# Kernel tuning notes

Measured on AMD Instinct MI355X. Metric: run time of the kernel, lower is better.

## Reference

```python
import jax, jax.numpy as jnp
import numpy as np

N_NODES = 100000
N_EDGES = 8192
DEG = 32                      # nodes per hyperedge
NNZ = N_EDGES * DEG
D_IN = 128
D_HID = 128
D_EDGE = 64
EPS = 1e-5


def _batchnorm(x, g, b):
    # normalize per-feature over the batch (dim 0), as a BatchNorm1d in train mode
    mu = jnp.mean(x, axis=0)
    var = jnp.var(x, axis=0)
    return (x - mu) * jax.lax.rsqrt(var + EPS) * g + b


def _hconv(x, src, eid, w, W, b):
    # hypergraph conv: linear -> node->edge weighted sum -> edge->node weighted sum
    h = x @ W + b                                          # [N, Dout]
    m = jax.ops.segment_sum(w[:, None] * h[src], eid, num_segments=N_EDGES)
    out = jax.ops.segment_sum(w[:, None] * m[eid], src, num_segments=N_NODES)
    return out


def setup_inputs() -> dict:
    key = jax.random.key(0)
    ks = jax.random.split(key, 20)
    src = jax.random.randint(ks[0], (NNZ,), 0, N_NODES)
    eid = jnp.arange(NNZ) // DEG                          # every edge id appears DEG times
    edge_index = jnp.stack([src, eid]).astype(jnp.int64)
    s = lambda k, sh, f: jax.random.normal(k, sh, jnp.float32) * f
    return {
        "x": s(ks[1], (N_NODES, D_IN), 1.0),
        "edge_index": edge_index,
        "edge_weight": jax.random.uniform(ks[2], (NNZ,), jnp.float32),
        "edge_features": s(ks[3], (N_EDGES, D_EDGE), 1.0),
        "adj": jax.random.uniform(ks[4], (N_EDGES, N_EDGES), jnp.float32) / N_EDGES,
        "T": 2,
        "norm1_g": jnp.ones((D_IN,), jnp.float32),
        "norm1_b": jnp.zeros((D_IN,), jnp.float32),
        "norm2_g": jnp.ones((D_EDGE,), jnp.float32),
        "norm2_b": jnp.zeros((D_EDGE,), jnp.float32),
        "W1": s(ks[5], (D_IN, D_HID), 0.05),
        "b1": jnp.zeros((D_HID,), jnp.float32),
        "W2": s(ks[6], (D_HID, D_HID), 0.05),
        "b2": jnp.zeros((D_HID,), jnp.float32),
        "Wn": s(ks[7], (D_HID, D_HID), 0.05),
        "We": s(ks[8], (D_EDGE, D_HID), 0.05),
        "Wg": s(ks[9], (D_HID, D_HID), 0.05),
        "cls_w1": s(ks[10], (D_HID, 16), 0.1),
        "cls_b1": jnp.zeros((16,), jnp.float32),
        "cls_w2": s(ks[11], (16, 2), 0.1),
        "cls_b2": jnp.zeros((2,), jnp.float32),
    }


def reference(x, edge_index, edge_weight, edge_features, adj, T,
              norm1_g, norm1_b, norm2_g, norm2_b,
              W1, b1, W2, b2, Wn, We, Wg,
              cls_w1, cls_b1, cls_w2, cls_b2):
    src, eid = edge_index[0], edge_index[1]
    x = _batchnorm(x, norm1_g, norm1_b)
    x = _hconv(x, src, eid, edge_weight, W1, b1)
    x = _hconv(x, src, eid, edge_weight, W2, b2)
    x = jax.nn.relu(x)
    # aggregate_node_features (mean over nodes incident to each hyperedge) —
    # the per-edge Python loop becomes one fused segment reduce
    s = jax.ops.segment_sum(x[src], eid, num_segments=N_EDGES)           # [E, D]
    cnt = jax.ops.segment_sum(jnp.ones_like(eid, jnp.float32), eid, num_segments=N_EDGES)
    node_features = s / jnp.maximum(cnt, 1.0)[:, None]
    ef = _batchnorm(edge_features, norm2_g, norm2_b)
    # edge-level graph convolution with T propagation steps over edge-edge adj
    h = jax.nn.relu(node_features @ Wn + ef @ We)
    for _ in range(T):
        h = jax.nn.relu(adj @ (h @ Wg))
    # classifier head
    out = jax.nn.relu(h @ cls_w1 + cls_b1) @ cls_w2 + cls_b2             # [E, 2]
    return out
```

## Files before the change

kernel.cpp:

```cpp
#include <hip/hip_runtime.h>

#define N_NODESC 100000
#define N_EDGESC 8192
#define DEGC 32
#define DF 128
#define DEF 64
#define EPSV 1e-5f
#define KSPLIT 8
#define KSLICE (N_EDGESC / KSPLIT)

#define NCVT 16384
#define NXST 400
#define NEST 64

typedef __attribute__((ext_vector_type(8))) short short8;
typedef __attribute__((ext_vector_type(4))) float f32x4;
typedef __attribute__((ext_vector_type(8))) unsigned short ushort8;
typedef __attribute__((ext_vector_type(4))) unsigned short u16x4;

typedef const void __attribute__((address_space(1)))* gptr_t;
typedef void __attribute__((address_space(3)))* lptr_t;

struct EW { int e; float w; };

__device__ __forceinline__ unsigned short f2bf(float x) {
    union { float f; unsigned u; } v; v.f = x;
    unsigned r = v.u + 0x7fffu + ((v.u >> 16) & 1u);
    return (unsigned short)(r >> 16);
}

__global__ __launch_bounds__(256) void fused_pre(const float* __restrict__ x,
                                                 const float* __restrict__ ef,
                                                 const int* __restrict__ src,
                                                 const float* __restrict__ ew,
                                                 const float* __restrict__ adj,
                                                 unsigned short* __restrict__ adjbf,
                                                 float* __restrict__ stats,
                                                 int* __restrict__ cnt,
                                                 EW* __restrict__ ewpk) {
    const int b = blockIdx.x;
    if (b < NCVT) {
        const size_t base4 = (size_t)b * 1024;
        const f32x4* in4 = (const f32x4*)adj + base4;
        u16x4* out4 = (u16x4*)adjbf + base4;
        f32x4 a[4];
        #pragma unroll
        for (int k = 0; k < 4; ++k) a[k] = in4[threadIdx.x + k * 256];
        #pragma unroll
        for (int k = 0; k < 4; ++k) {
            u16x4 r;
            r[0] = f2bf(a[k][0]); r[1] = f2bf(a[k][1]);
            r[2] = f2bf(a[k][2]); r[3] = f2bf(a[k][3]);
            out4[threadIdx.x + k * 256] = r;
        }
        return;
    }
    const int bs = b - NCVT;
    if (bs >= NXST + NEST) {
        int i = (bs - NXST - NEST) * 256 + threadIdx.x;
        int n = src[i];
        int pos = atomicAdd(&cnt[n], 1);
        if (pos < DEGC) {
            EW t; t.e = i >> 5; t.w = ew[i];
            ewpk[(size_t)n * DEGC + pos] = t;
        }
        return;
    }
    __shared__ f32x4 ls[256], lq[256];
    if (bs < NXST) {
        const int q = threadIdx.x & 31, rg = threadIdx.x >> 5;
        f32x4 s = {0.f, 0.f, 0.f, 0.f}, s2 = {0.f, 0.f, 0.f, 0.f};
        for (int r = bs * 8 + rg; r < N_NODESC; r += NXST * 8) {
            f32x4 v = *(const f32x4*)&x[(size_t)r * DF + q * 4];
            s += v; s2 += v * v;
        }
        ls[threadIdx.x] = s; lq[threadIdx.x] = s2;
        __syncthreads();
        if (threadIdx.x < 32) {
            #pragma unroll
            for (int g = 1; g < 8; ++g) { s += ls[threadIdx.x + g * 32]; s2 += lq[threadIdx.x + g * 32]; }
            #pragma unroll
            for (int i = 0; i < 4; ++i) {
                atomicAdd(&stats[q * 4 + i], s[i]);
                atomicAdd(&stats[128 + q * 4 + i], s2[i]);
            }
        }
    } else {
        const int bb = bs - NXST;
        const int q = threadIdx.x & 15, rg = threadIdx.x >> 4;
        f32x4 s = {0.f, 0.f, 0.f, 0.f}, s2 = {0.f, 0.f, 0.f, 0.f};
        for (int r = bb * 16 + rg; r < N_EDGESC; r += NEST * 16) {
            f32x4 v = *(const f32x4*)&ef[(size_t)r * DEF + q * 4];
            s += v; s2 += v * v;
        }
        ls[threadIdx.x] = s; lq[threadIdx.x] = s2;
        __syncthreads();
        if (threadIdx.x < 16) {
            #pragma unroll
            for (int g = 1; g < 16; ++g) { s += ls[threadIdx.x + g * 16]; s2 += lq[threadIdx.x + g * 16]; }
            #pragma unroll
            for (int i = 0; i < 4; ++i) {
                atomicAdd(&stats[512 + q * 4 + i], s[i]);
                atomicAdd(&stats[576 + q * 4 + i], s2[i]);
            }
        }
    }
}

__global__ void finalize_both(const float* __restrict__ stats,
                              const float* __restrict__ g1, const float* __restrict__ b1,
                              const float* __restrict__ g2, const float* __restrict__ b2,
                              float* __restrict__ ssx, float* __restrict__ sse) {
    int t = threadIdx.x;
    if (t < 128) {
        float mean = stats[t] / (float)N_NODESC;
        float var = stats[128 + t] / (float)N_NODESC - mean * mean;
        float sc = g1[t] * rsqrtf(var + EPSV);
        ssx[t] = sc;
        ssx[128 + t] = b1[t] - mean * sc;
    } else {
        int f = t - 128;
        float mean = stats[512 + f] / (float)N_EDGESC;
        float var = stats[576 + f] / (float)N_EDGESC - mean * mean;
        float sc = g2[f] * rsqrtf(var + EPSV);
        sse[f] = sc;
        sse[64 + f] = b2[f] - mean * sc;
    }
}

__global__ __launch_bounds__(256) void node_apply(const float* __restrict__ m,
                                                  const int* __restrict__ cnt,
                                                  const EW* __restrict__ ewpk,
                                                  float* __restrict__ out) {
    const int n = blockIdx.x * 2 + (threadIdx.x >> 7);
    const int f = threadIdx.x & 127;
    if (n >= N_NODESC) return;
    int d = cnt[n];
    if (d <= 0) return;
    d = min(d, DEGC);
    const EW* q = ewpk + (size_t)n * DEGC;
    float acc = 0.f;
    for (int p = 0; p < d; ++p) {
        EW t = q[p];
        acc += t.w * m[(size_t)t.e * DF + f];
    }
    out[(size_t)n * DF + f] = acc;
}

template<bool WEIGHTED, bool AFFINE, bool RELU, bool WRITE_SW>
__global__ __launch_bounds__(128) void gather_k(const float* __restrict__ X,
                                                const float* __restrict__ w,
                                                const int* __restrict__ src,
                                                const float* __restrict__ scale,
                                                const float* __restrict__ shift,
                                                float* __restrict__ out,
                                                float* __restrict__ swout,
                                                float mul) {
    const int e = blockIdx.x, f = threadIdx.x;
    const int base = e * DEGC;
    float acc = 0.f, sw = 0.f;
    #pragma unroll
    for (int j = 0; j < DEGC; ++j) {
        int n = src[base + j];
        float wj = WEIGHTED ? w[base + j] : 1.f;
        float v = X[(size_t)n * DF + f];
        if (RELU) v = fmaxf(v, 0.f);
        acc += wj * v;
        sw += wj;
    }
    float r = acc;
    if (AFFINE) r = acc * scale[f] + sw * shift[f];
    out[(size_t)e * DF + f] = r * mul;
    if (WRITE_SW && f == 0) swout[e] = sw;
}

template<int K1, int K2, int NSLICE, bool RELU_IN, bool RELU_OUT, bool BIAS>
__global__ __launch_bounds__(256) void egemm(const float* __restrict__ A1, const float* __restrict__ W1p,
                                             const float* __restrict__ A2, const float* __restrict__ W2p,
                                             const float* __restrict__ sc2, const float* __restrict__ sh2,
                                             const float* __restrict__ bias, const float* __restrict__ swv,
                                             float* __restrict__ C) {
    constexpr int P1 = K1 + 4;
    constexpr int K2c = (K2 > 0) ? K2 : 1;
    constexpr int P2 = K2c + 4;
    constexpr size_t SLSTR = (size_t)N_EDGESC * K1;
    __shared__ float wt1[DF * P1];
    __shared__ float a1c[32 * K1];
    __shared__ float wt2[(K2 > 0) ? DF * P2 : 1];
    __shared__ float a2c[(K2 > 0) ? 32 * K2c : 1];

    const int tid = threadIdx.x;
    const int r0 = blockIdx.x * 32;

    for (int idx = tid; idx < K1 * DF; idx += 256) {
        int k = idx >> 7, c = idx & 127;
        wt1[c * P1 + k] = W1p[idx];
    }
    for (int idx = tid; idx < 32 * K1; idx += 256) {
        float v;
        if constexpr (NSLICE > 1) {
            v = 0.f;
            #pragma unroll
            for (int s = 0; s < NSLICE; ++s) v += A1[s * SLSTR + (size_t)r0 * K1 + idx];
        } else {
            v = A1[(size_t)r0 * K1 + idx];
        }
        if (RELU_IN) v = fmaxf(v, 0.f);
        a1c[idx] = v;
    }
    if constexpr (K2 > 0) {
        for (int idx = tid; idx < K2 * DF; idx += 256) {
            int k = idx >> 7, c = idx & 127;
            wt2[c * P2 + k] = W2p[idx];
        }
        for (int idx = tid; idx < 32 * K2; idx += 256) {
            int k = idx % K2;
            a2c[idx] = A2[(size_t)r0 * K2 + idx] * sc2[k] + sh2[k];
        }
    }
    __syncthreads();

    const int cg = tid & 31, rg = tid >> 5;
    float acc[4][4];
    if constexpr (BIAS) {
        float bl[4], sl[4];
        #pragma unroll
        for (int j = 0; j < 4; ++j) bl[j] = bias[cg * 4 + j];
        #pragma unroll
        for (int i = 0; i < 4; ++i) sl[i] = swv[r0 + rg * 4 + i];
        #pragma unroll
        for (int i = 0; i < 4; ++i)
            #pragma unroll
            for (int j = 0; j < 4; ++j) acc[i][j] = sl[i] * bl[j];
    } else {
        #pragma unroll
        for (int i = 0; i < 4; ++i)
            #pragma unroll
            for (int j = 0; j < 4; ++j) acc[i][j] = 0.f;
    }

    #pragma unroll 4
    for (int k4 = 0; k4 < K1; k4 += 4) {
        f32x4 av[4], wv[4];
        #pragma unroll
        for (int i = 0; i < 4; ++i) av[i] = *(const f32x4*)&a1c[(rg * 4 + i) * K1 + k4];
        #pragma unroll
        for (int j = 0; j < 4; ++j) wv[j] = *(const f32x4*)&wt1[(cg * 4 + j) * P1 + k4];
        #pragma unroll
        for (int i = 0; i < 4; ++i)
            #pragma unroll
            for (int j = 0; j < 4; ++j)
                #pragma unroll
                for (int q = 0; q < 4; ++q) acc[i][j] += av[i][q] * wv[j][q];
    }
    if constexpr (K2 > 0) {
        #pragma unroll 4
        for (int k4 = 0; k4 < K2; k4 += 4) {
            f32x4 av[4], wv[4];
            #pragma unroll
            for (int i = 0; i < 4; ++i) av[i] = *(const f32x4*)&a2c[(rg * 4 + i) * K2c + k4];
            #pragma unroll
            for (int j = 0; j < 4; ++j) wv[j] = *(const f32x4*)&wt2[(cg * 4 + j) * P2 + k4];
            #pragma unroll
            for (int i = 0; i < 4; ++i)
                #pragma unroll
                for (int j = 0; j < 4; ++j)
                    #pragma unroll
                    for (int q = 0; q < 4; ++q) acc[i][j] += av[i][q] * wv[j][q];
        }
    }

    #pragma unroll
    for (int i = 0; i < 4; ++i) {
        f32x4 o;
        #pragma unroll
        for (int j = 0; j < 4; ++j) {
            float v = acc[i][j];
            if (RELU_OUT) v = fmaxf(v, 0.f);
            o[j] = v;
        }
        *(f32x4*)&C[(size_t)(r0 + rg * 4 + i) * DF + cg * 4] = o;
    }
}

__global__ __launch_bounds__(256) void transp_cvt(const float* __restrict__ Y,
                                                  unsigned short* __restrict__ Yt) {
    __shared__ float t[32][33];
    const int r0 = blockIdx.x * 32, c0 = blockIdx.y * 32;
    const int tc = threadIdx.x & 31, tr = threadIdx.x >> 5;
    #pragma unroll
    for (int i = 0; i < 4; ++i)
        t[tr + i * 8][tc] = Y[(size_t)(r0 + tr + i * 8) * DF + c0 + tc];
    __syncthreads();
    #pragma unroll
    for (int i = 0; i < 4; ++i) {
        int c = tr + i * 8;
        Yt[(size_t)(c0 + c) * N_EDGESC + r0 + tc] = f2bf(t[tc][c]);
    }
}

__global__ __launch_bounds__(256, 2) void adj_gemm(const unsigned short* __restrict__ A,
                                                   const unsigned short* __restrict__ Bt,
                                                   float* __restrict__ H) {
    __shared__ unsigned short sA[2][128 * 64];
    __shared__ unsigned short sB[2][128 * 64];
    const int tid = threadIdx.x;
    const int lane = tid & 63, wave = tid >> 6;
    const int mb = blockIdx.x & 63, ks = blockIdx.x >> 6;
    const size_t m0 = (size_t)mb * 128;
    const int k0 = ks * KSLICE;
    const int wm = wave >> 1, wn = wave & 1;
    float* __restrict__ Hs = H + (size_t)ks * (N_EDGESC * DF);

    f32x4 acc[4][4];
    #pragma unroll
    for (int i = 0; i < 4; ++i)
        #pragma unroll
        for (int j = 0; j < 4; ++j) acc[i][j] = 0.f;

    auto stage = [&](int buf, int kc) {
        #pragma unroll
        for (int i = 0; i < 4; ++i) {
            int slot = i * 256 + wave * 64 + lane;
            int row = slot >> 3, ch = slot & 7;
            int sc = (ch ^ (row & 7)) << 3;
            const unsigned short* ga = A + (m0 + row) * (size_t)N_EDGESC + kc + sc;
            const unsigned short* gb = Bt + (size_t)row * N_EDGESC + kc + sc;
            unsigned short* la = &sA[buf][(i * 256 + wave * 64) * 8];
            unsigned short* lb = &sB[buf][(i * 256 + wave * 64) * 8];
            __builtin_amdgcn_global_load_lds((gptr_t)ga, (lptr_t)la, 16, 0, 0);
            __builtin_amdgcn_global_load_lds((gptr_t)gb, (lptr_t)lb, 16, 0, 0);
        }
    };

    stage(0, k0);
    int cur = 0;
    for (int c = 0; c < KSLICE / 64; ++c) {
        __syncthreads();
        if (c + 1 < KSLICE / 64) stage(cur ^ 1, k0 + (c + 1) * 64);
        #pragma unroll
        for (int kk = 0; kk < 2; ++kk) {
            short8 af[4], bv[4];
            const int chb = kk * 4 + (lane >> 4);
            #pragma unroll
            for (int mf = 0; mf < 4; ++mf) {
                int row = wm * 64 + mf * 16 + (lane & 15);
                af[mf] = *(const short8*)&sA[cur][(row * 8 + (chb ^ (row & 7))) * 8];
            }
            #pragma unroll
            for (int nf = 0; nf < 4; ++nf) {
                int row = wn * 64 + nf * 16 + (lane & 15);
                bv[nf] = *(const short8*)&sB[cur][(row * 8 + (chb ^ (row & 7))) * 8];
            }
            #pragma unroll
            for (int mf = 0; mf < 4; ++mf)
                #pragma unroll
                for (int nf = 0; nf < 4; ++nf)
                    acc[mf][nf] = __builtin_amdgcn_mfma_f32_16x16x32_bf16(af[mf], bv[nf], acc[mf][nf], 0, 0, 0);
        }
        cur ^= 1;
    }

    #pragma unroll
    for (int mf = 0; mf < 4; ++mf)
        #pragma unroll
        for (int nf = 0; nf < 4; ++nf)
            #pragma unroll
            for (int r = 0; r < 4; ++r) {
                size_t row = m0 + wm * 64 + mf * 16 + (lane >> 4) * 4 + r;
                int col = wn * 64 + nf * 16 + (lane & 15);
                Hs[row * DF + col] = acc[mf][nf][r];
            }
}

__global__ __launch_bounds__(256) void classifier_k(const float* __restrict__ H,
                                                    const float* __restrict__ w1, const float* __restrict__ b1,
                                                    const float* __restrict__ w2, const float* __restrict__ b2,
                                                    float* __restrict__ out) {
    constexpr size_t SLSTR = (size_t)N_EDGESC * DF;
    __shared__ float hl[16 * DF];
    __shared__ float w1l[DF * 16];
    __shared__ float hid[16 * 16];
    const int tid = threadIdx.x;
    const int e0 = blockIdx.x * 16;
    for (int idx = tid; idx < 16 * DF; idx += 256) {
        float v = 0.f;
        #pragma unroll
        for (int s = 0; s < KSPLIT; ++s) v += H[s * SLSTR + (size_t)e0 * DF + idx];
        hl[idx] = fmaxf(v, 0.f);
    }
    for (int idx = tid; idx < DF * 16; idx += 256) w1l[idx] = w1[idx];
    __syncthreads();
    {
        int el = tid >> 4, j = tid & 15;
        float a = b1[j];
        for (int k = 0; k < DF; ++k) a += hl[el * DF + k] * w1l[k * 16 + j];
        hid[el * 16 + j] = fmaxf(a, 0.f);
    }
    __syncthreads();
    if (tid < 32) {
        int e = tid >> 1, o = tid & 1;
        float s = b2[o];
        for (int jj = 0; jj < 16; ++jj) s += hid[e * 16 + jj] * w2[jj * 2 + o];
        out[(size_t)(e0 + e) * 2 + o] = s;
    }
}

extern "C" void kernel_launch(void* const* d_in, const int* in_sizes, int n_in,
                              void* d_out, int out_size, void* d_ws, size_t ws_size,
                              hipStream_t stream) {
    const float* x   = (const float*)d_in[0];
    const int*  src  = (const int*)d_in[1];
    const float* ew  = (const float*)d_in[2];
    const float* ef  = (const float*)d_in[3];
    const float* adj = (const float*)d_in[4];
    const float* n1g = (const float*)d_in[6];
    const float* n1b = (const float*)d_in[7];
    const float* n2g = (const float*)d_in[8];
    const float* n2b = (const float*)d_in[9];
    const float* W1  = (const float*)d_in[10];
    const float* b1  = (const float*)d_in[11];
    const float* W2  = (const float*)d_in[12];
    const float* b2  = (const float*)d_in[13];
    const float* Wn  = (const float*)d_in[14];
    const float* We  = (const float*)d_in[15];
    const float* Wg  = (const float*)d_in[16];
    const float* cw1 = (const float*)d_in[17];
    const float* cb1 = (const float*)d_in[18];
    const float* cw2 = (const float*)d_in[19];
    const float* cb2 = (const float*)d_in[20];
    float* out = (float*)d_out;

    float* stats  = (float*)d_ws;
    float* ssx    = stats + 256;
    float* sse    = stats + 640;
    float* sw     = stats + 1024;
    int*   cnt    = (int*)(sw + 8192);
    EW*    ewpk   = (EW*)(cnt + N_NODESC);
    float* EB0    = (float*)(ewpk + (size_t)N_NODESC * DEGC);
    float* EB1    = EB0 + (size_t)N_EDGESC * DF;
    float* HS     = EB1 + (size_t)N_EDGESC * DF;
    float* NODES  = HS + (size_t)KSPLIT * N_EDGESC * DF;
    unsigned short* yT    = (unsigned short*)(NODES + (size_t)N_NODESC * DF);
    unsigned short* adjbf = yT + (size_t)DF * N_EDGESC;

    (void)hipMemsetAsync(stats, 0, (1024 + 8192) * sizeof(float) + N_NODESC * sizeof(int), stream);

    fused_pre<<<NCVT + NXST + NEST + (N_EDGESC * DEGC) / 256, 256, 0, stream>>>(
        x, ef, src, ew, adj, adjbf, stats, cnt, ewpk);
    finalize_both<<<1, 192, 0, stream>>>(stats, n1g, n1b, n2g, n2b, ssx, sse);

    gather_k<true, true, false, true><<<N_EDGESC, 128, 0, stream>>>(x, ew, src, ssx, ssx + 128, EB0, sw, 1.f);
    egemm<128, 0, 1, false, false, true><<<256, 256, 0, stream>>>(EB0, W1, nullptr, nullptr, nullptr, nullptr, b1, sw, EB1);
    node_apply<<<N_NODESC / 2, 256, 0, stream>>>(EB1, cnt, ewpk, NODES);

    gather_k<true, false, false, false><<<N_EDGESC, 128, 0, stream>>>(NODES, ew, src, nullptr, nullptr, EB0, nullptr, 1.f);
    egemm<128, 0, 1, false, false, true><<<256, 256, 0, stream>>>(EB0, W2, nullptr, nullptr, nullptr, nullptr, b2, sw, EB1);
    node_apply<<<N_NODESC / 2, 256, 0, stream>>>(EB1, cnt, ewpk, NODES);

    gather_k<false, false, true, false><<<N_EDGESC, 128, 0, stream>>>(NODES, nullptr, src, nullptr, nullptr, EB0, nullptr, 1.f / DEGC);

    egemm<128, 64, 1, false, true, false><<<256, 256, 0, stream>>>(EB0, Wn, ef, We, sse, sse + 64, nullptr, nullptr, EB1);

    egemm<128, 0, 1, false, false, false><<<256, 256, 0, stream>>>(EB1, Wg, nullptr, nullptr, nullptr, nullptr, nullptr, nullptr, EB0);
    transp_cvt<<<dim3(256, 4), 256, 0, stream>>>(EB0, yT);
    adj_gemm<<<64 * KSPLIT, 256, 0, stream>>>(adjbf, yT, HS);
    egemm<128, 0, KSPLIT, true, false, false><<<256, 256, 0, stream>>>(HS, Wg, nullptr, nullptr, nullptr, nullptr, nullptr, nullptr, EB0);
    transp_cvt<<<dim3(256, 4), 256, 0, stream>>>(EB0, yT);
    adj_gemm<<<64 * KSPLIT, 256, 0, stream>>>(adjbf, yT, HS);

    classifier_k<<<N_EDGESC / 16, 256, 0, stream>>>(HS, cw1, cb1, cw2, cb2, out);
}
```

Before: 492.3 us.

## Spread adj bf16 conversion across gather/node kernels and fold BN finalize into consumers

The 16384-block fp32-to-bf16 conversion of the adjacency matrix is moved out of the up-front pre-pass. It is split into five chunks of 3277 blocks, each prepended to one of the memory-latency-bound gather_k and node_apply launches so it can overlap with their gathers. The finalize_both kernel is removed: BN scale and shift are computed inline in gather_k for x and in egemm for edge features. gather_k also handles two edges per 256-thread block. This saves one launch and tries to hide conversion bandwidth, at the cost of mixing streaming and gather blocks in each launch.

```diff
diff --git a/kernel.cpp b/kernel.cpp
--- a/kernel.cpp
+++ b/kernel.cpp
@@ -9,7 +9,8 @@
 #define KSPLIT 8
 #define KSLICE (N_EDGESC / KSPLIT)
 
-#define NCVT 16384
+#define NCVT_TOT 16384
+#define CVS 3277
 #define NXST 400
 #define NEST 64
 
@@ -29,35 +30,34 @@
     return (unsigned short)(r >> 16);
 }
 
-__global__ __launch_bounds__(256) void fused_pre(const float* __restrict__ x,
+__device__ __forceinline__ void cvt_block(int cb, const float* __restrict__ adj,
+                                          unsigned short* __restrict__ adjbf) {
+    if (cb >= NCVT_TOT) return;
+    const size_t base4 = (size_t)cb * 1024;
+    const f32x4* in4 = (const f32x4*)adj + base4;
+    u16x4* out4 = (u16x4*)adjbf + base4;
+    f32x4 a[4];
+    #pragma unroll
+    for (int k = 0; k < 4; ++k) a[k] = in4[threadIdx.x + k * 256];
+    #pragma unroll
+    for (int k = 0; k < 4; ++k) {
+        u16x4 r;
+        r[0] = f2bf(a[k][0]); r[1] = f2bf(a[k][1]);
+        r[2] = f2bf(a[k][2]); r[3] = f2bf(a[k][3]);
+        out4[threadIdx.x + k * 256] = r;
+    }
+}
+
+__global__ __launch_bounds__(256) void pre_small(const float* __restrict__ x,
                                                  const float* __restrict__ ef,
                                                  const int* __restrict__ src,
                                                  const float* __restrict__ ew,
-                                                 const float* __restrict__ adj,
-                                                 unsigned short* __restrict__ adjbf,
                                                  float* __restrict__ stats,
                                                  int* __restrict__ cnt,
                                                  EW* __restrict__ ewpk) {
     const int b = blockIdx.x;
-    if (b < NCVT) {
-        const size_t base4 = (size_t)b * 1024;
-        const f32x4* in4 = (const f32x4*)adj + base4;
-        u16x4* out4 = (u16x4*)adjbf + base4;
-        f32x4 a[4];
-        #pragma unroll
-        for (int k = 0; k < 4; ++k) a[k] = in4[threadIdx.x + k * 256];
-        #pragma unroll
-        for (int k = 0; k < 4; ++k) {
-            u16x4 r;
-            r[0] = f2bf(a[k][0]); r[1] = f2bf(a[k][1]);
-            r[2] = f2bf(a[k][2]); r[3] = f2bf(a[k][3]);
-            out4[threadIdx.x + k * 256] = r;
-        }
-        return;
-    }
-    const int bs = b - NCVT;
-    if (bs >= NXST + NEST) {
-        int i = (bs - NXST - NEST) * 256 + threadIdx.x;
+    if (b >= NXST + NEST) {
+        int i = (b - NXST - NEST) * 256 + threadIdx.x;
         int n = src[i];
         int pos = atomicAdd(&cnt[n], 1);
         if (pos < DEGC) {
@@ -67,10 +67,10 @@
         return;
     }
     __shared__ f32x4 ls[256], lq[256];
-    if (bs < NXST) {
+    if (b < NXST) {
         const int q = threadIdx.x & 31, rg = threadIdx.x >> 5;
         f32x4 s = {0.f, 0.f, 0.f, 0.f}, s2 = {0.f, 0.f, 0.f, 0.f};
-        for (int r = bs * 8 + rg; r < N_NODESC; r += NXST * 8) {
+        for (int r = b * 8 + rg; r < N_NODESC; r += NXST * 8) {
             f32x4 v = *(const f32x4*)&x[(size_t)r * DF + q * 4];
             s += v; s2 += v * v;
         }
@@ -86,7 +86,7 @@
             }
         }
     } else {
-        const int bb = bs - NXST;
+        const int bb = b - NXST;
         const int q = threadIdx.x & 15, rg = threadIdx.x >> 4;
         f32x4 s = {0.f, 0.f, 0.f, 0.f}, s2 = {0.f, 0.f, 0.f, 0.f};
         for (int r = bb * 16 + rg; r < N_EDGESC; r += NEST * 16) {
@@ -107,32 +107,17 @@
     }
 }
 
-__global__ void finalize_both(const float* __restrict__ stats,
-                              const float* __restrict__ g1, const float* __restrict__ b1,
-                              const float* __restrict__ g2, const float* __restrict__ b2,
-                              float* __restrict__ ssx, float* __restrict__ sse) {
-    int t = threadIdx.x;
-    if (t < 128) {
-        float mean = stats[t] / (float)N_NODESC;
-        float var = stats[128 + t] / (float)N_NODESC - mean * mean;
-        float sc = g1[t] * rsqrtf(var + EPSV);
-        ssx[t] = sc;
-        ssx[128 + t] = b1[t] - mean * sc;
-    } else {
-        int f = t - 128;
-        float mean = stats[512 + f] / (float)N_EDGESC;
-        float var = stats[576 + f] / (float)N_EDGESC - mean * mean;
-        float sc = g2[f] * rsqrtf(var + EPSV);
-        sse[f] = sc;
-        sse[64 + f] = b2[f] - mean * sc;
-    }
-}
-
 __global__ __launch_bounds__(256) void node_apply(const float* __restrict__ m,
                                                   const int* __restrict__ cnt,
                                                   const EW* __restrict__ ewpk,
-                                                  float* __restrict__ out) {
-    const int n = blockIdx.x * 2 + (threadIdx.x >> 7);
+                                                  float* __restrict__ out,
+                                                  const float* __restrict__ adj,
+                                                  unsigned short* __restrict__ adjbf,
+                                                  int cvtBase) {
+    int b = blockIdx.x;
+    if (b < CVS) { cvt_block(cvtBase + b, adj, adjbf); return; }
+    b -= CVS;
+    const int n = b * 2 + (threadIdx.x >> 7);
     const int f = threadIdx.x & 127;
     if (n >= N_NODESC) return;
     int d = cnt[n];
@@ -148,15 +133,30 @@
 }
 
 template<bool WEIGHTED, bool AFFINE, bool RELU, bool WRITE_SW>
-__global__ __launch_bounds__(128) void gather_k(const float* __restrict__ X,
+__global__ __launch_bounds__(256) void gather_k(const float* __restrict__ X,
                                                 const float* __restrict__ w,
                                                 const int* __restrict__ src,
-                                                const float* __restrict__ scale,
-                                                const float* __restrict__ shift,
+                                                const float* __restrict__ stats,
+                                                const float* __restrict__ g1,
+                                                const float* __restrict__ b1,
                                                 float* __restrict__ out,
                                                 float* __restrict__ swout,
-                                                float mul) {
-    const int e = blockIdx.x, f = threadIdx.x;
+                                                float mul,
+                                                const float* __restrict__ adj,
+                                                unsigned short* __restrict__ adjbf,
+                                                int cvtBase) {
+    int b = blockIdx.x;
+    if (b < CVS) { cvt_block(cvtBase + b, adj, adjbf); return; }
+    b -= CVS;
+    const int e = b * 2 + (threadIdx.x >> 7);
+    const int f = threadIdx.x & 127;
+    float scale = 1.f, shift = 0.f;
+    if (AFFINE) {
+        float mean = stats[f] / (float)N_NODESC;
+        float var = stats[128 + f] / (float)N_NODESC - mean * mean;
+        scale = g1[f] * rsqrtf(var + EPSV);
+        shift = b1[f] - mean * scale;
+    }
     const int base = e * DEGC;
     float acc = 0.f, sw = 0.f;
     #pragma unroll
@@ -169,7 +169,7 @@
         sw += wj;
     }
     float r = acc;
-    if (AFFINE) r = acc * scale[f] + sw * shift[f];
+    if (AFFINE) r = acc * scale + sw * shift;
     out[(size_t)e * DF + f] = r * mul;
     if (WRITE_SW && f == 0) swout[e] = sw;
 }
@@ -177,7 +177,8 @@
 template<int K1, int K2, int NSLICE, bool RELU_IN, bool RELU_OUT, bool BIAS>
 __global__ __launch_bounds__(256) void egemm(const float* __restrict__ A1, const float* __restrict__ W1p,
                                              const float* __restrict__ A2, const float* __restrict__ W2p,
-                                             const float* __restrict__ sc2, const float* __restrict__ sh2,
+                                             const float* __restrict__ statsE, const float* __restrict__ g2,
+                                             const float* __restrict__ b2v, float cntE,
                                              const float* __restrict__ bias, const float* __restrict__ swv,
                                              float* __restrict__ C) {
     constexpr int P1 = K1 + 4;
@@ -188,9 +189,21 @@
     __shared__ float a1c[32 * K1];
     __shared__ float wt2[(K2 > 0) ? DF * P2 : 1];
     __shared__ float a2c[(K2 > 0) ? 32 * K2c : 1];
+    __shared__ float sseL[(K2 > 0) ? 2 * K2c : 1];
 
     const int tid = threadIdx.x;
     const int r0 = blockIdx.x * 32;
+
+    if constexpr (K2 > 0) {
+        if (tid < K2) {
+            float mean = statsE[tid] / cntE;
+            float var = statsE[K2 + tid] / cntE - mean * mean;
+            float sc = g2[tid] * rsqrtf(var + EPSV);
+            sseL[tid] = sc;
+            sseL[K2 + tid] = b2v[tid] - mean * sc;
+        }
+        __syncthreads();
+    }
 
     for (int idx = tid; idx < K1 * DF; idx += 256) {
         int k = idx >> 7, c = idx & 127;
@@ -215,7 +228,7 @@
         }
         for (int idx = tid; idx < 32 * K2; idx += 256) {
             int k = idx % K2;
-            a2c[idx] = A2[(size_t)r0 * K2 + idx] * sc2[k] + sh2[k];
+            a2c[idx] = A2[(size_t)r0 * K2 + idx] * sseL[k] + sseL[K2 + k];
         }
     }
     __syncthreads();
@@ -432,8 +445,6 @@
     float* out = (float*)d_out;
 
     float* stats  = (float*)d_ws;
-    float* ssx    = stats + 256;
-    float* sse    = stats + 640;
     float* sw     = stats + 1024;
     int*   cnt    = (int*)(sw + 8192);
     EW*    ewpk   = (EW*)(cnt + N_NODESC);
@@ -446,26 +457,33 @@
 
     (void)hipMemsetAsync(stats, 0, (1024 + 8192) * sizeof(float) + N_NODESC * sizeof(int), stream);
 
-    fused_pre<<<NCVT + NXST + NEST + (N_EDGESC * DEGC) / 256, 256, 0, stream>>>(
-        x, ef, src, ew, adj, adjbf, stats, cnt, ewpk);
-    finalize_both<<<1, 192, 0, stream>>>(stats, n1g, n1b, n2g, n2b, ssx, sse);
-
-    gather_k<true, true, false, true><<<N_EDGESC, 128, 0, stream>>>(x, ew, src, ssx, ssx + 128, EB0, sw, 1.f);
-    egemm<128, 0, 1, false, false, true><<<256, 256, 0, stream>>>(EB0, W1, nullptr, nullptr, nullptr, nullptr, b1, sw, EB1);
-    node_apply<<<N_NODESC / 2, 256, 0, stream>>>(EB1, cnt, ewpk, NODES);
-
-    gather_k<true, false, false, false><<<N_EDGESC, 128, 0, stream>>>(NODES, ew, src, nullptr, nullptr, EB0, nullptr, 1.f);
-    egemm<128, 0, 1, false, false, true><<<256, 256, 0, stream>>>(EB0, W2, nullptr, nullptr, nullptr, nullptr, b2, sw, EB1);
-    node_apply<<<N_NODESC / 2, 256, 0, stream>>>(EB1, cnt, ewpk, NODES);
-
-    gather_k<false, false, true, false><<<N_EDGESC, 128, 0, stream>>>(NODES, nullptr, src, nullptr, nullptr, EB0, nullptr, 1.f / DEGC);
-
-    egemm<128, 64, 1, false, true, false><<<256, 256, 0, stream>>>(EB0, Wn, ef, We, sse, sse + 64, nullptr, nullptr, EB1);
-
-    egemm<128, 0, 1, false, false, false><<<256, 256, 0, stream>>>(EB1, Wg, nullptr, nullptr, nullptr, nullptr, nullptr, nullptr, EB0);
+    pre_small<<<NXST + NEST + (N_EDGESC * DEGC) / 256, 256, 0, stream>>>(
+        x, ef, src, ew, stats, cnt, ewpk);
+
+    gather_k<true, true, false, true><<<CVS + N_EDGESC / 2, 256, 0, stream>>>(
+        x, ew, src, stats, n1g, n1b, EB0, sw, 1.f, adj, adjbf, 0);
+    egemm<128, 0, 1, false, false, true><<<256, 256, 0, stream>>>(
+        EB0, W1, nullptr, nullptr, nullptr, nullptr, nullptr, 1.f, b1, sw, EB1);
+    node_apply<<<CVS + N_NODESC / 2, 256, 0, stream>>>(EB1, cnt, ewpk, NODES, adj, adjbf, CVS);
+
+    gather_k<true, false, false, false><<<CVS + N_EDGESC / 2, 256, 0, stream>>>(
+        NODES, ew, src, nullptr, nullptr, nullptr, EB0, nullptr, 1.f, adj, adjbf, 2 * CVS);
+    egemm<128, 0, 1, false, false, true><<<256, 256, 0, stream>>>(
+        EB0, W2, nullptr, nullptr, nullptr, nullptr, nullptr, 1.f, b2, sw, EB1);
+    node_apply<<<CVS + N_NODESC / 2, 256, 0, stream>>>(EB1, cnt, ewpk, NODES, adj, adjbf, 3 * CVS);
+
+    gather_k<false, false, true, false><<<CVS + N_EDGESC / 2, 256, 0, stream>>>(
+        NODES, nullptr, src, nullptr, nullptr, nullptr, EB0, nullptr, 1.f / DEGC, adj, adjbf, 4 * CVS);
+
+    egemm<128, 64, 1, false, true, false><<<256, 256, 0, stream>>>(
+        EB0, Wn, ef, We, stats + 512, n2g, n2b, (float)N_EDGESC, nullptr, nullptr, EB1);
+
+    egemm<128, 0, 1, false, false, false><<<256, 256, 0, stream>>>(
+        EB1, Wg, nullptr, nullptr, nullptr, nullptr, nullptr, 1.f, nullptr, nullptr, EB0);
     transp_cvt<<<dim3(256, 4), 256, 0, stream>>>(EB0, yT);
     adj_gemm<<<64 * KSPLIT, 256, 0, stream>>>(adjbf, yT, HS);
-    egemm<128, 0, KSPLIT, true, false, false><<<256, 256, 0, stream>>>(HS, Wg, nullptr, nullptr, nullptr, nullptr, nullptr, nullptr, EB0);
+    egemm<128, 0, KSPLIT, true, false, false><<<256, 256, 0, stream>>>(
+        HS, Wg, nullptr, nullptr, nullptr, nullptr, nullptr, 1.f, nullptr, nullptr, EB0);
     transp_cvt<<<dim3(256, 4), 256, 0, stream>>>(EB0, yT);
     adj_gemm<<<64 * KSPLIT, 256, 0, stream>>>(adjbf, yT, HS);
 
```

Measured after the change: 502.6 us. +2.1%, slower.
